# Optimization experiments

Hardware: AMD Instinct MI355X
Metric: run time of the kernel (lower is better)

Reference implementation:

```python
import jax, jax.numpy as jnp
import numpy as np

V, E, H, B, S = 50000, 256, 256, 64, 2048


def setup_inputs() -> dict:
    key = jax.random.key(0)
    ks = jax.random.split(key, 13)
    u = lambda k, shape: jax.random.uniform(k, shape, jnp.float32) - 0.5
    return {
        "inp": jax.random.randint(ks[0], (B,), 0, V, dtype=jnp.int64),
        "hidden": jax.random.normal(ks[1], (1, B, H), jnp.float32),
        "encoder_outputs": jax.random.normal(ks[2], (B, S, H), jnp.float32),
        "emb": jax.random.normal(ks[3], (V, E), jnp.float32),          # nn.Embedding weight
        "U": u(ks[4], (H, H)),
        "W": u(ks[5], (H, H)),
        "v": u(ks[6], (H, 1)),
        "W_ih": u(ks[7], (H, E)),   # RNN weight_ih_l0
        "W_hh": u(ks[8], (H, H)),   # RNN weight_hh_l0
        "b_ih": u(ks[9], (H,)),
        "b_hh": u(ks[10], (H,)),
        "W_out": u(ks[11], (V, H)),  # output Linear weight
        "b_out": u(ks[12], (V,)),
    }


def reference(inp, hidden, encoder_outputs, emb, U, W, v,
              W_ih, W_hh, b_ih, b_hh, W_out, b_out):
    # embedding lookup: (B, E)
    x = emb[inp]
    word_embs = x[:, None, :]                         # (B, 1, E)
    # Bahdanau additive attention (get_context)
    summed = jnp.tanh(word_embs @ U + encoder_outputs @ W)   # (B, S, H)
    e_ij = summed @ v                                        # (B, S, 1)
    alpha = jax.nn.softmax(e_ij, axis=1)                     # (B, S, 1)
    context = jnp.sum(alpha * encoder_outputs, axis=1)       # (B, H)
    # single tanh-RNN step; NOTE: original code feeds context as initial hidden,
    # ignoring the `hidden` argument when attention is enabled.
    h_new = jnp.tanh(x @ W_ih.T + b_ih + context @ W_hh.T + b_hh)  # (B, H)
    logits = h_new @ W_out.T + b_out                               # (B, V)
    return logits, h_new[None]                                     # hidden: (1, B, H)
```

## Files before the change

kernel.cpp:

```cpp
#include <hip/hip_runtime.h>
#include <hip/hip_bf16.h>
#include <math.h>

#define V_ 50000
#define E_ 256
#define H_ 256
#define B_ 64
#define S_ 2048
#define NCHK 32

typedef __attribute__((ext_vector_type(4))) float f32x4;
typedef __attribute__((ext_vector_type(16))) float f32x16;
typedef __attribute__((ext_vector_type(8))) __bf16 bf16x8;

static __device__ __forceinline__ f32x4 mfma16(bf16x8 a, bf16x8 b, f32x4 c) {
  return __builtin_amdgcn_mfma_f32_16x16x32_bf16(a, b, c, 0, 0, 0);
}
static __device__ __forceinline__ f32x16 mfma32(bf16x8 a, bf16x8 b, f32x16 c) {
  return __builtin_amdgcn_mfma_f32_32x32x16_bf16(a, b, c, 0, 0, 0);
}
static __device__ __forceinline__ float fast_tanh(float x) {
  const float e2 = __expf(2.0f * x);
  return 1.0f - 2.0f / (e2 + 1.0f);
}
static __device__ __forceinline__ void gll16(const float* g, void* l) {
  __builtin_amdgcn_global_load_lds(
      (const __attribute__((address_space(1))) void*)g,
      (__attribute__((address_space(3))) void*)l, 16, 0, 0);
}

__global__ __launch_bounds__(256) void prep_k(
    const int* __restrict__ inp, const float* __restrict__ emb,
    const float* __restrict__ U, const float* __restrict__ W_ih,
    const float* __restrict__ b_ih, const float* __restrict__ b_hh,
    float* __restrict__ xU, float* __restrict__ xWih) {
  const int b = blockIdx.x, h = threadIdx.x;
  __shared__ float xs[H_];
  xs[h] = emb[(size_t)inp[b] * E_ + h];
  __syncthreads();
  float au = 0.f, aw = 0.f;
  const float* __restrict__ wir = W_ih + (size_t)h * E_;
  for (int k = 0; k < H_; k += 4) {
    const float4 x4 = *reinterpret_cast<const float4*>(&xs[k]);
    const float4 w4 = *reinterpret_cast<const float4*>(wir + k);
    aw = fmaf(x4.x, w4.x, aw); aw = fmaf(x4.y, w4.y, aw);
    aw = fmaf(x4.z, w4.z, aw); aw = fmaf(x4.w, w4.w, aw);
    au = fmaf(x4.x, U[(size_t)(k + 0) * H_ + h], au);
    au = fmaf(x4.y, U[(size_t)(k + 1) * H_ + h], au);
    au = fmaf(x4.z, U[(size_t)(k + 2) * H_ + h], au);
    au = fmaf(x4.w, U[(size_t)(k + 3) * H_ + h], au);
  }
  xU[b * H_ + h] = au;
  xWih[b * H_ + h] = aw + b_ih[h] + b_hh[h];
}

__global__ __launch_bounds__(256) void prep_w(
    const float* __restrict__ W, __bf16* __restrict__ wt2) {
  const int idx = blockIdx.x * 256 + threadIdx.x;
  const int k = idx >> 8, col = idx & 255;
  wt2[((size_t)(k >> 3) * 256 + col) * 8 + (k & 7)] = (__bf16)W[(size_t)k * H_ + col];
}

#define SLAB 4096
__global__ __launch_bounds__(256, 3) void attn_fused(
    const float* __restrict__ enc, const __bf16* __restrict__ wt2,
    const float* __restrict__ xU, const float* __restrict__ vv,
    float* __restrict__ ctxp, float* __restrict__ mlout) {
  const int t = threadIdx.x;
  const int w = t >> 6, l = t & 63, l31 = l & 31, h5 = l >> 5;
  const int rg = w >> 1, cg = w & 1;

  __shared__ __align__(16) char Aring[4 * SLAB];
  __shared__ float ered[2][64];
  __shared__ float wgt[64];
  __shared__ float mlS[2];

  const int ridx = blockIdx.x;
  const int b = blockIdx.y;
  const int s0 = ridx * 64;

  const int srow = w * 16 + (l >> 2);
  const int pch = l & 3;
  const int kch = pch ^ ((srow >> 1) & 3);
  const float* __restrict__ encSrc = enc + ((size_t)b * S_ + s0 + srow) * H_ + kch * 4;

#define STAGE(ks_)                                                   \
  gll16(encSrc + (ks_) * 16, Aring + ((ks_) & 3) * SLAB + w * 1024); \
  __builtin_amdgcn_sched_barrier(0);

  STAGE(0); STAGE(1); STAGE(2);
  bf16x8 bh[2][4], bl2[2][4];
#pragma unroll
  for (int cf = 0; cf < 4; ++cf) {
    const int col = cg * 128 + cf * 32 + l31;
    bh[0][cf] = *reinterpret_cast<const bf16x8*>(wt2 + ((size_t)h5 * 256 + col) * 8);
  }

  f32x16 acc[4];
#pragma unroll
  for (int cf = 0; cf < 4; ++cf) acc[cf] = (f32x16)(0.f);

  const int r = rg * 32 + l31;
  const int sxor = (r >> 1) & 3;
  const char* arow = Aring + r * 64;

#pragma unroll
  for (int ks = 0; ks < 16; ++ks) {
    if (ks <= 13)      asm volatile("s_waitcnt vmcnt(6)" ::: "memory");
    else if (ks == 14) asm volatile("s_waitcnt vmcnt(5)" ::: "memory");
    else               asm volatile("s_waitcnt vmcnt(4)" ::: "memory");
    __builtin_amdgcn_s_barrier();
    __builtin_amdgcn_sched_barrier(0);
    if (ks <= 12) { STAGE(ks + 3); }
    const int pb = ks & 1;
    if (ks < 15) {
      const int koct = (ks + 1) * 2 + h5;
#pragma unroll
      for (int cf = 0; cf < 4; ++cf) {
        const int col = cg * 128 + cf * 32 + l31;
        bh[pb ^ 1][cf] = *reinterpret_cast<const bf16x8*>(
            wt2 + ((size_t)koct * 256 + col) * 8);
      }
    }
    const char* sb = arow + (ks & 3) * SLAB;
    const f32x4 c0 = *reinterpret_cast<const f32x4*>(sb + (((2 * h5 + 0) ^ sxor) << 4));
    const f32x4 c1 = *reinterpret_cast<const f32x4*>(sb + (((2 * h5 + 1) ^ sxor) << 4));
    bf16x8 ahi, alo;
    {
      const float xa[8] = {c0[0], c0[1], c0[2], c0[3], c1[0], c1[1], c1[2], c1[3]};
#pragma unroll
      for (int j = 0; j < 8; ++j) {
        const __bf16 hh = (__bf16)xa[j];
        ahi[j] = hh;
        alo[j] = (__bf16)(xa[j] - (float)hh);
      }
    }
#pragma unroll
    for (int cf = 0; cf < 4; ++cf) acc[cf] = mfma32(ahi, bh[pb][cf], acc[cf]);
#pragma unroll
    for (int cf = 0; cf < 4; ++cf) acc[cf] = mfma32(alo, bh[pb][cf], acc[cf]);
  }
#undef STAGE

  float xu[4], vw[4];
#pragma unroll
  for (int cf = 0; cf < 4; ++cf) {
    const int col = cg * 128 + cf * 32 + l31;
    xu[cf] = xU[b * H_ + col];
    vw[cf] = vv[col];
  }
  float rs[16];
#pragma unroll
  for (int reg = 0; reg < 16; ++reg) {
    float s = 0.f;
#pragma unroll
    for (int cf = 0; cf < 4; ++cf)
      s += fast_tanh(xu[cf] + acc[cf][reg]) * vw[cf];
    rs[reg] = s;
  }
#pragma unroll
  for (int o = 1; o < 32; o <<= 1)
#pragma unroll
    for (int reg = 0; reg < 16; ++reg)
      rs[reg] += __shfl_xor(rs[reg], o);
  if (l31 == 0) {
#pragma unroll
    for (int reg = 0; reg < 16; ++reg)
      ered[cg][rg * 32 + (reg & 3) + 8 * (reg >> 2) + 4 * h5] = rs[reg];
  }
  __syncthreads();

  if (t < 64) {
    const float es = ered[0][t] + ered[1][t];
    float m = es;
#pragma unroll
    for (int o = 1; o < 64; o <<= 1) m = fmaxf(m, __shfl_xor(m, o));
    const float we = __expf(es - m);
    float ls = we;
#pragma unroll
    for (int o = 1; o < 64; o <<= 1) ls += __shfl_xor(ls, o);
    wgt[t] = we;
    if (t == 0) { mlS[0] = m; mlS[1] = ls; }
  }
  __syncthreads();

  {
    const float* __restrict__ ep = enc + ((size_t)b * S_ + s0) * H_ + t;
    float a = 0.f;
#pragma unroll 8
    for (int s = 0; s < 64; ++s) a = fmaf(wgt[s], ep[(size_t)s * H_], a);
    ctxp[((size_t)ridx * B_ + b) * H_ + t] = a;
  }
  if (t < 2) mlout[(ridx * B_ + b) * 2 + t] = mlS[t];
}

__global__ __launch_bounds__(256) void combine_hnew(
    const float* __restrict__ ctxp, const float* __restrict__ mlout,
    const float* __restrict__ xWih, const float* __restrict__ W_hh,
    float* __restrict__ out_h, __bf16* __restrict__ hn) {
  const int b = blockIdx.x, h = threadIdx.x;
  __shared__ float cs[H_];
  float M = -3.4e38f;
#pragma unroll
  for (int cc = 0; cc < NCHK; ++cc) M = fmaxf(M, mlout[(cc * B_ + b) * 2]);
  float num = 0.f, den = 0.f;
#pragma unroll
  for (int cc = 0; cc < NCHK; ++cc) {
    const float mw = __expf(mlout[(cc * B_ + b) * 2] - M);
    den = fmaf(mw, mlout[(cc * B_ + b) * 2 + 1], den);
    num = fmaf(mw, ctxp[((size_t)cc * B_ + b) * H_ + h], num);
  }
  cs[h] = num / den;
  __syncthreads();
  const float* __restrict__ wr = W_hh + (size_t)h * H_;
  float a = xWih[b * H_ + h];
  for (int k = 0; k < H_; k += 4) {
    const float4 w4 = *reinterpret_cast<const float4*>(wr + k);
    const float4 c4 = *reinterpret_cast<const float4*>(&cs[k]);
    a = fmaf(c4.x, w4.x, a); a = fmaf(c4.y, w4.y, a);
    a = fmaf(c4.z, w4.z, a); a = fmaf(c4.w, w4.w, a);
  }
  const float hv = fast_tanh(a);
  out_h[b * H_ + h] = hv;
  hn[b * H_ + h] = (__bf16)hv;
}

__global__ __launch_bounds__(256) void logits_mfma(
    const float* __restrict__ Wout, const float* __restrict__ bout,
    const __bf16* __restrict__ hn, float* __restrict__ logits) {
  const int v0 = blockIdx.x * 64;
  const int t = threadIdx.x;
  const int wv = t >> 6, l = t & 63, l15 = l & 15, lg = l >> 4;

  __shared__ __bf16 Wsub[8][64][32];

  {
    const int srow = t >> 2, sg = t & 3;
    const int wslot = (sg + (srow >> 1)) & 3;
    const int vc = (v0 + srow) < V_ ? (v0 + srow) : (V_ - 1);
    const float* __restrict__ wr = Wout + (size_t)vc * H_ + sg * 8;
#pragma unroll
    for (int ks = 0; ks < 8; ++ks) {
      const float4 f0 = *reinterpret_cast<const float4*>(wr + ks * 32);
      const float4 f1 = *reinterpret_cast<const float4*>(wr + ks * 32 + 4);
      const float xv[8] = {f0.x, f0.y, f0.z, f0.w, f1.x, f1.y, f1.z, f1.w};
      bf16x8 h8;
#pragma unroll
      for (int j = 0; j < 8; ++j) h8[j] = (__bf16)xv[j];
      *reinterpret_cast<bf16x8*>(&Wsub[ks][srow][wslot * 8]) = h8;
    }
  }
  __syncthreads();

  f32x4 acc[4];
#pragma unroll
  for (int i = 0; i < 4; ++i) acc[i] = (f32x4)(0.f);
  const int colb = wv * 16 + l15;
#pragma unroll
  for (int k = 0; k < 8; ++k) {
    const bf16x8 bfrag = *reinterpret_cast<const bf16x8*>(hn + (size_t)colb * H_ + k * 32 + lg * 8);
    bf16x8 ah[4];
#pragma unroll
    for (int rf = 0; rf < 4; ++rf) {
      const int rr = rf * 16 + l15;
      const int slot = (lg + (rr >> 1)) & 3;
      ah[rf] = *reinterpret_cast<const bf16x8*>(&Wsub[k][rr][slot * 8]);
    }
#pragma unroll
    for (int rf = 0; rf < 4; ++rf)
      acc[rf] = mfma16(ah[rf], bfrag, acc[rf]);
  }
#pragma unroll
  for (int rf = 0; rf < 4; ++rf) {
    const int v = v0 + rf * 16 + lg * 4;
    if (v < V_) {
      const float4 bo = *reinterpret_cast<const float4*>(bout + v);
      float4 o;
      o.x = acc[rf][0] + bo.x; o.y = acc[rf][1] + bo.y;
      o.z = acc[rf][2] + bo.z; o.w = acc[rf][3] + bo.w;
      *reinterpret_cast<float4*>(logits + (size_t)colb * V_ + v) = o;
    }
  }
}

extern "C" void kernel_launch(void* const* d_in, const int* in_sizes, int n_in,
                              void* d_out, int out_size, void* d_ws, size_t ws_size,
                              hipStream_t stream) {
  const int*   inp  = (const int*)  d_in[0];
  const float* enc  = (const float*)d_in[2];
  const float* emb  = (const float*)d_in[3];
  const float* U    = (const float*)d_in[4];
  const float* W    = (const float*)d_in[5];
  const float* v    = (const float*)d_in[6];
  const float* W_ih = (const float*)d_in[7];
  const float* W_hh = (const float*)d_in[8];
  const float* b_ih = (const float*)d_in[9];
  const float* b_hh = (const float*)d_in[10];
  const float* Wout = (const float*)d_in[11];
  const float* bout = (const float*)d_in[12];

  float* logits = (float*)d_out;
  float* out_h  = logits + (size_t)B_ * V_;

  float* ws    = (float*)d_ws;
  __bf16* wt2  = (__bf16*)ws;
  float* xU    = ws + 32768;
  float* xWih  = xU + B_ * H_;
  float* ctxp  = xWih + B_ * H_;
  float* mlout = ctxp + (size_t)NCHK * B_ * H_;
  __bf16* hn   = (__bf16*)(mlout + NCHK * B_ * 2);

  prep_k<<<dim3(B_), dim3(256), 0, stream>>>(inp, emb, U, W_ih, b_ih, b_hh, xU, xWih);
  prep_w<<<dim3(H_ * H_ / 256), dim3(256), 0, stream>>>(W, wt2);
  attn_fused<<<dim3(NCHK, B_), dim3(256), 0, stream>>>(enc, wt2, xU, v, ctxp, mlout);
  combine_hnew<<<dim3(B_), dim3(256), 0, stream>>>(ctxp, mlout, xWih, W_hh, out_h, hn);
  logits_mfma<<<dim3((V_ + 63) / 64), dim3(256), 0, stream>>>(Wout, bout, hn, logits);
}
```

Baseline: 105.4 us.

## Give each wave a private LDS ring to drop block barriers in attention GEMM

Each wave now stages its own 32 encoder rows into a private 8 KB LDS ring using two direct-to-LDS loads per stage. The per-iteration workgroup s_barrier is removed and replaced by per-wave vmcnt waits. The xU and v loads are hoisted ahead of the pipeline so they overlap the main loop. The cost is 4x more LDS (32 KB), which may limit occupancy under launch_bounds(256,3), and each pair of waves sharing a row group loads the encoder data redundantly.

```diff
diff --git a/kernel.cpp b/kernel.cpp
--- a/kernel.cpp
+++ b/kernel.cpp
@@ -61,7 +61,7 @@
   wt2[((size_t)(k >> 3) * 256 + col) * 8 + (k & 7)] = (__bf16)W[(size_t)k * H_ + col];
 }
 
-#define SLAB 4096
+#define WRING 8192
 __global__ __launch_bounds__(256, 3) void attn_fused(
     const float* __restrict__ enc, const __bf16* __restrict__ wt2,
     const float* __restrict__ xU, const float* __restrict__ vv,
@@ -70,7 +70,7 @@
   const int w = t >> 6, l = t & 63, l31 = l & 31, h5 = l >> 5;
   const int rg = w >> 1, cg = w & 1;
 
-  __shared__ __align__(16) char Aring[4 * SLAB];
+  __shared__ __align__(16) char Aring[4 * WRING];
   __shared__ float ered[2][64];
   __shared__ float wgt[64];
   __shared__ float mlS[2];
@@ -79,37 +79,44 @@
   const int b = blockIdx.y;
   const int s0 = ridx * 64;
 
-  const int srow = w * 16 + (l >> 2);
-  const int pch = l & 3;
-  const int kch = pch ^ ((srow >> 1) & 3);
-  const float* __restrict__ encSrc = enc + ((size_t)b * S_ + s0 + srow) * H_ + kch * 4;
-
-#define STAGE(ks_)                                                   \
-  gll16(encSrc + (ks_) * 16, Aring + ((ks_) & 3) * SLAB + w * 1024); \
+  float xu[4], vw[4];
+#pragma unroll
+  for (int cf = 0; cf < 4; ++cf) {
+    const int col = cg * 128 + cf * 32 + l31;
+    xu[cf] = xU[b * H_ + col];
+    vw[cf] = vv[col];
+  }
   __builtin_amdgcn_sched_barrier(0);
 
+  const float* __restrict__ encSrc =
+      enc + ((size_t)b * S_ + s0 + rg * 32 + (l & 31)) * H_ + (l >> 5) * 4;
+  char* __restrict__ ring = Aring + w * WRING;
+
+#define STAGE(ks_)                                                    \
+  gll16(encSrc + (ks_) * 16,     ring + ((ks_) & 3) * 2048);          \
+  gll16(encSrc + (ks_) * 16 + 8, ring + ((ks_) & 3) * 2048 + 1024);   \
+  __builtin_amdgcn_sched_barrier(0);
+
   STAGE(0); STAGE(1); STAGE(2);
-  bf16x8 bh[2][4], bl2[2][4];
+  bf16x8 bh[2][4];
 #pragma unroll
   for (int cf = 0; cf < 4; ++cf) {
     const int col = cg * 128 + cf * 32 + l31;
     bh[0][cf] = *reinterpret_cast<const bf16x8*>(wt2 + ((size_t)h5 * 256 + col) * 8);
   }
+  __builtin_amdgcn_sched_barrier(0);
 
   f32x16 acc[4];
 #pragma unroll
   for (int cf = 0; cf < 4; ++cf) acc[cf] = (f32x16)(0.f);
 
-  const int r = rg * 32 + l31;
-  const int sxor = (r >> 1) & 3;
-  const char* arow = Aring + r * 64;
-
 #pragma unroll
   for (int ks = 0; ks < 16; ++ks) {
-    if (ks <= 13)      asm volatile("s_waitcnt vmcnt(6)" ::: "memory");
-    else if (ks == 14) asm volatile("s_waitcnt vmcnt(5)" ::: "memory");
-    else               asm volatile("s_waitcnt vmcnt(4)" ::: "memory");
-    __builtin_amdgcn_s_barrier();
+    if (ks == 0)       asm volatile("s_waitcnt vmcnt(8)" ::: "memory");
+    else if (ks == 1)  asm volatile("s_waitcnt vmcnt(12)" ::: "memory");
+    else if (ks <= 13) asm volatile("s_waitcnt vmcnt(16)" ::: "memory");
+    else if (ks == 14) asm volatile("s_waitcnt vmcnt(14)" ::: "memory");
+    else               asm volatile("s_waitcnt vmcnt(12)" ::: "memory");
     __builtin_amdgcn_sched_barrier(0);
     if (ks <= 12) { STAGE(ks + 3); }
     const int pb = ks & 1;
@@ -122,9 +129,9 @@
             wt2 + ((size_t)koct * 256 + col) * 8);
       }
     }
-    const char* sb = arow + (ks & 3) * SLAB;
-    const f32x4 c0 = *reinterpret_cast<const f32x4*>(sb + (((2 * h5 + 0) ^ sxor) << 4));
-    const f32x4 c1 = *reinterpret_cast<const f32x4*>(sb + (((2 * h5 + 1) ^ sxor) << 4));
+    const char* sb = ring + (ks & 3) * 2048 + h5 * 1024 + l31 * 16;
+    const f32x4 c0 = *reinterpret_cast<const f32x4*>(sb);
+    const f32x4 c1 = *reinterpret_cast<const f32x4*>(sb + 512);
     bf16x8 ahi, alo;
     {
       const float xa[8] = {c0[0], c0[1], c0[2], c0[3], c1[0], c1[1], c1[2], c1[3]};
@@ -142,13 +149,6 @@
   }
 #undef STAGE
 
-  float xu[4], vw[4];
-#pragma unroll
-  for (int cf = 0; cf < 4; ++cf) {
-    const int col = cg * 128 + cf * 32 + l31;
-    xu[cf] = xU[b * H_ + col];
-    vw[cf] = vv[col];
-  }
   float rs[16];
 #pragma unroll
   for (int reg = 0; reg < 16; ++reg) {
```

Result: slower. 112.6 us (+6.9%).

## Deepen encoder staging ring to 8 slabs and process two k-steps per barrier

Applied to the files above, without the earlier changes.

Expands the LDS ring for encoder tiles from 4 to 8 slabs. Each barrier-separated iteration now handles two k-steps, with six stages prefetched up front and two new stages issued per iteration. It also swaps the round-to-nearest bf16 hi/lo split for a truncation-based split done with byte-permute instructions, which lowers conversion ALU work. The goal is fewer barriers and more loads in flight. The cost is double the LDS use, which may limit occupancy, along with more registers for B fragments and a slightly different hi/lo split.

```diff
diff --git a/kernel.cpp b/kernel.cpp
--- a/kernel.cpp
+++ b/kernel.cpp
@@ -27,6 +27,22 @@
   __builtin_amdgcn_global_load_lds(
       (const __attribute__((address_space(1))) void*)g,
       (__attribute__((address_space(3))) void*)l, 16, 0, 0);
+}
+static __device__ __forceinline__ void cvt_hilo(
+    const f32x4 c0, const f32x4 c1, bf16x8& ahi, bf16x8& alo) {
+  union U { bf16x8 v; unsigned u[4]; } H, L;
+  const float x[8] = {c0[0], c0[1], c0[2], c0[3], c1[0], c1[1], c1[2], c1[3]};
+#pragma unroll
+  for (int p = 0; p < 4; ++p) {
+    const unsigned a0 = __float_as_uint(x[2 * p]);
+    const unsigned a1 = __float_as_uint(x[2 * p + 1]);
+    H.u[p] = __builtin_amdgcn_perm(a1, a0, 0x07060302);
+    const float l0 = x[2 * p]     - __uint_as_float(a0 & 0xFFFF0000u);
+    const float l1 = x[2 * p + 1] - __uint_as_float(a1 & 0xFFFF0000u);
+    L.u[p] = __builtin_amdgcn_perm(__float_as_uint(l1), __float_as_uint(l0), 0x07060302);
+  }
+  ahi = H.v;
+  alo = L.v;
 }
 
 __global__ __launch_bounds__(256) void prep_k(
@@ -61,7 +77,6 @@
   wt2[((size_t)(k >> 3) * 256 + col) * 8 + (k & 7)] = (__bf16)W[(size_t)k * H_ + col];
 }
 
-#define SLAB 4096
 __global__ __launch_bounds__(256, 3) void attn_fused(
     const float* __restrict__ enc, const __bf16* __restrict__ wt2,
     const float* __restrict__ xU, const float* __restrict__ vv,
@@ -70,7 +85,7 @@
   const int w = t >> 6, l = t & 63, l31 = l & 31, h5 = l >> 5;
   const int rg = w >> 1, cg = w & 1;
 
-  __shared__ __align__(16) char Aring[4 * SLAB];
+  __shared__ __align__(16) char Aring[8 * 4096];
   __shared__ float ered[2][64];
   __shared__ float wgt[64];
   __shared__ float mlS[2];
@@ -79,22 +94,26 @@
   const int b = blockIdx.y;
   const int s0 = ridx * 64;
 
-  const int srow = w * 16 + (l >> 2);
-  const int pch = l & 3;
+  const int srow = t >> 2;
+  const int pch = t & 3;
   const int kch = pch ^ ((srow >> 1) & 3);
   const float* __restrict__ encSrc = enc + ((size_t)b * S_ + s0 + srow) * H_ + kch * 4;
 
 #define STAGE(ks_)                                                   \
-  gll16(encSrc + (ks_) * 16, Aring + ((ks_) & 3) * SLAB + w * 1024); \
+  gll16(encSrc + (ks_) * 16, Aring + ((ks_) & 7) * 4096 + w * 1024); \
   __builtin_amdgcn_sched_barrier(0);
 
-  STAGE(0); STAGE(1); STAGE(2);
-  bf16x8 bh[2][4], bl2[2][4];
-#pragma unroll
-  for (int cf = 0; cf < 4; ++cf) {
-    const int col = cg * 128 + cf * 32 + l31;
-    bh[0][cf] = *reinterpret_cast<const bf16x8*>(wt2 + ((size_t)h5 * 256 + col) * 8);
-  }
+  STAGE(0); STAGE(1); STAGE(2); STAGE(3); STAGE(4); STAGE(5);
+  bf16x8 bh[2][2][4];
+#pragma unroll
+  for (int hh = 0; hh < 2; ++hh)
+#pragma unroll
+    for (int cf = 0; cf < 4; ++cf) {
+      const int col = cg * 128 + cf * 32 + l31;
+      bh[0][hh][cf] = *reinterpret_cast<const bf16x8*>(
+          wt2 + ((size_t)(hh * 2 + h5) * 256 + col) * 8);
+    }
+  __builtin_amdgcn_sched_barrier(0);
 
   f32x16 acc[4];
 #pragma unroll
@@ -105,40 +124,42 @@
   const char* arow = Aring + r * 64;
 
 #pragma unroll
-  for (int ks = 0; ks < 16; ++ks) {
-    if (ks <= 13)      asm volatile("s_waitcnt vmcnt(6)" ::: "memory");
-    else if (ks == 14) asm volatile("s_waitcnt vmcnt(5)" ::: "memory");
-    else               asm volatile("s_waitcnt vmcnt(4)" ::: "memory");
+  for (int it = 0; it < 8; ++it) {
+    if (it == 0)      asm volatile("s_waitcnt vmcnt(12)" ::: "memory");
+    else if (it == 1) asm volatile("s_waitcnt vmcnt(20)" ::: "memory");
+    else if (it <= 5) asm volatile("s_waitcnt vmcnt(28)" ::: "memory");
+    else if (it == 6) asm volatile("s_waitcnt vmcnt(26)" ::: "memory");
+    else              asm volatile("s_waitcnt vmcnt(24)" ::: "memory");
     __builtin_amdgcn_s_barrier();
     __builtin_amdgcn_sched_barrier(0);
-    if (ks <= 12) { STAGE(ks + 3); }
-    const int pb = ks & 1;
-    if (ks < 15) {
-      const int koct = (ks + 1) * 2 + h5;
-#pragma unroll
-      for (int cf = 0; cf < 4; ++cf) {
-        const int col = cg * 128 + cf * 32 + l31;
-        bh[pb ^ 1][cf] = *reinterpret_cast<const bf16x8*>(
-            wt2 + ((size_t)koct * 256 + col) * 8);
+    if (it <= 4) { STAGE(2 * it + 6); STAGE(2 * it + 7); }
+    const int pb = it & 1;
+    if (it < 7) {
+#pragma unroll
+      for (int hh = 0; hh < 2; ++hh) {
+        const int koct = (2 * (it + 1) + hh) * 2 + h5;
+#pragma unroll
+        for (int cf = 0; cf < 4; ++cf) {
+          const int col = cg * 128 + cf * 32 + l31;
+          bh[pb ^ 1][hh][cf] = *reinterpret_cast<const bf16x8*>(
+              wt2 + ((size_t)koct * 256 + col) * 8);
+        }
       }
     }
-    const char* sb = arow + (ks & 3) * SLAB;
-    const f32x4 c0 = *reinterpret_cast<const f32x4*>(sb + (((2 * h5 + 0) ^ sxor) << 4));
-    const f32x4 c1 = *reinterpret_cast<const f32x4*>(sb + (((2 * h5 + 1) ^ sxor) << 4));
-    bf16x8 ahi, alo;
-    {
-      const float xa[8] = {c0[0], c0[1], c0[2], c0[3], c1[0], c1[1], c1[2], c1[3]};
-#pragma unroll
-      for (int j = 0; j < 8; ++j) {
-        const __bf16 hh = (__bf16)xa[j];
-        ahi[j] = hh;
-        alo[j] = (__bf16)(xa[j] - (float)hh);
-      }
-    }
-#pragma unroll
-    for (int cf = 0; cf < 4; ++cf) acc[cf] = mfma32(ahi, bh[pb][cf], acc[cf]);
-#pragma unroll
-    for (int cf = 0; cf < 4; ++cf) acc[cf] = mfma32(alo, bh[pb][cf], acc[cf]);
+    __builtin_amdgcn_sched_barrier(0);
+#pragma unroll
+    for (int hh = 0; hh < 2; ++hh) {
+      const int ks = 2 * it + hh;
+      const char* sb = arow + (ks & 7) * 4096;
+      const f32x4 c0 = *reinterpret_cast<const f32x4*>(sb + (((2 * h5 + 0) ^ sxor) << 4));
+      const f32x4 c1 = *reinterpret_cast<const f32x4*>(sb + (((2 * h5 + 1) ^ sxor) << 4));
+      bf16x8 ahi, alo;
+      cvt_hilo(c0, c1, ahi, alo);
+#pragma unroll
+      for (int cf = 0; cf < 4; ++cf) acc[cf] = mfma32(ahi, bh[pb][hh][cf], acc[cf]);
+#pragma unroll
+      for (int cf = 0; cf < 4; ++cf) acc[cf] = mfma32(alo, bh[pb][hh][cf], acc[cf]);
+    }
   }
 #undef STAGE
 
```

Result: faster. 102.2 us (-3.0%).
